# Optimization experiments

Measured on AMD Instinct MI355X. Metric: run time of the kernel, lower is better.

Reference implementation:

```python
import jax, jax.numpy as jnp
import numpy as np

B, S, D, H = 2, 2048, 1024, 16
HD = D // H  # head_dim = 64
SCALE = HD ** -0.5


def setup_inputs() -> dict:
    key = jax.random.key(0)
    ks = jax.random.split(key, 10)
    std = D ** -0.5
    return {
        "x": jax.random.normal(ks[0], (B, S, D), jnp.float32),
        "y": jax.random.normal(ks[1], (B, S, D), jnp.float32),
        "Wq": jax.random.normal(ks[2], (D, D), jnp.float32) * std,
        "bq": jnp.zeros((D,), jnp.float32),
        "Wk": jax.random.normal(ks[3], (D, D), jnp.float32) * std,
        "bk": jnp.zeros((D,), jnp.float32),
        "Wv": jax.random.normal(ks[4], (D, D), jnp.float32) * std,
        "bv": jnp.zeros((D,), jnp.float32),
        "Wo": jax.random.normal(ks[5], (D, D), jnp.float32) * std,
        "bo": jnp.zeros((D,), jnp.float32),
    }


def reference(x, y, Wq, bq, Wk, bk, Wv, bv, Wo, bo):
    # Linear projections (torch Linear: x @ W.T + b; here W stored as [in,out])
    q = x @ Wq + bq  # [B,S,D]
    k = y @ Wk + bk
    v = y @ Wv + bv
    # split heads -> [B,H,S,hd]
    q = q.reshape(B, S, H, HD).transpose(0, 2, 1, 3)
    k = k.reshape(B, S, H, HD).transpose(0, 2, 1, 3)
    v = v.reshape(B, S, H, HD).transpose(0, 2, 1, 3)
    scores = jnp.einsum("bhqd,bhkd->bhqk", q, k) * SCALE  # [B,H,S,S]
    causal = jnp.tril(jnp.ones((S, S), dtype=bool))  # keep lower triangle
    scores = jnp.where(causal[None, None], scores, -jnp.inf)
    attn = jax.nn.softmax(scores, axis=-1)
    out = jnp.einsum("bhqk,bhkd->bhqd", attn, v)  # [B,H,S,hd]
    out = out.transpose(0, 2, 1, 3).reshape(B, S, D)
    return out @ Wo + bo
```

## Files before the change

kernel.cpp:

```cpp
#include <hip/hip_runtime.h>
#include <hip/hip_bf16.h>


#define BDIM 2
#define SDIM 2048
#define DDIM 1024
#define HDIM 16
#define HD   64
#define MDIM (BDIM*SDIM)
#define C2 0.18033688011112042f

using short8  = __attribute__((ext_vector_type(8))) short;
using floatx4 = __attribute__((ext_vector_type(4))) float;

static __device__ __forceinline__ unsigned short f2bf(float x) {
    union { float f; unsigned int u; } c; c.f = x;
    unsigned int r = (c.u + 0x7fffu + ((c.u >> 16) & 1u)) >> 16;
    return (unsigned short)r;
}

static __device__ __forceinline__ unsigned int pack2bf(float a, float b) {
    union { float f; unsigned int u; } ua, ub;
    ua.f = a; ub.f = b;
    return __builtin_amdgcn_perm(ub.u + 0x8000u, ua.u + 0x8000u, 0x07060302u);
}

#define GLD16(g, l) __builtin_amdgcn_global_load_lds(                        \
    (const __attribute__((address_space(1))) void*)(g),                      \
    (__attribute__((address_space(3))) void*)(l), 16, 0, 0)

__global__ __launch_bounds__(256) void prep_kernel(
    const float* __restrict__ X, const float* __restrict__ Y,
    const float* __restrict__ W0, const float* __restrict__ W1,
    const float* __restrict__ W2, const float* __restrict__ W3,
    unsigned short* __restrict__ Xo, unsigned short* __restrict__ Yo,
    unsigned short* __restrict__ T0, unsigned short* __restrict__ T1,
    unsigned short* __restrict__ T2, unsigned short* __restrict__ T3)
{
    __shared__ float tile[64][68];
    const int z = blockIdx.z;
    const int t = threadIdx.x;
    if (z < 2) {
        const float* A    = z ? Y : X;
        unsigned short* O = z ? Yo : Xo;
        const int idx = blockIdx.x * 256 + t;
        const float4 a = ((const float4*)A)[idx*2];
        const float4 b = ((const float4*)A)[idx*2 + 1];
        ushort4 lo, hi;
        lo.x = f2bf(a.x); lo.y = f2bf(a.y); lo.z = f2bf(a.z); lo.w = f2bf(a.w);
        hi.x = f2bf(b.x); hi.y = f2bf(b.y); hi.z = f2bf(b.z); hi.w = f2bf(b.w);
        ((ushort4*)O)[idx*2]     = lo;
        ((ushort4*)O)[idx*2 + 1] = hi;
        return;
    }
    if (blockIdx.x >= 256) return;
    const int zz = z - 2;
    const float* W    = (zz == 0) ? W0 : (zz == 1) ? W1 : (zz == 2) ? W2 : W3;
    unsigned short* T = (zz == 0) ? T0 : (zz == 1) ? T1 : (zz == 2) ? T2 : T3;
    const int k0 = (blockIdx.x & 15) * 64, n0 = (blockIdx.x >> 4) * 64;
    #pragma unroll
    for (int i = 0; i < 4; ++i) {
        const int idx = t + i*256;
        const int kr = idx >> 4, c4 = idx & 15;
        float4 v = *(const float4*)&W[(size_t)(k0 + kr) * DDIM + n0 + c4*4];
        tile[kr][c4*4+0] = v.x; tile[kr][c4*4+1] = v.y;
        tile[kr][c4*4+2] = v.z; tile[kr][c4*4+3] = v.w;
    }
    __syncthreads();
    #pragma unroll
    for (int i = 0; i < 4; ++i) {
        const int idx = t + i*256;
        const int nr = idx >> 4, kc = idx & 15;
        ushort4 o;
        o.x = f2bf(tile[kc*4+0][nr]); o.y = f2bf(tile[kc*4+1][nr]);
        o.z = f2bf(tile[kc*4+2][nr]); o.w = f2bf(tile[kc*4+3][nr]);
        *(ushort4*)&T[(size_t)(n0 + nr) * DDIM + k0 + kc*4] = o;
    }
}

template <bool SWAP>
__device__ __forceinline__ void gemm128_core(
    const unsigned short* __restrict__ A, const unsigned short* __restrict__ Bt,
    int bm, int bn, unsigned short* As, unsigned short* Bs, floatx4 acc[4][4])
{
    const int t = threadIdx.x;
    const int w = t >> 6, l = t & 63;
    const int quad = l >> 4, col = l & 15;
    const int wr = (w >> 1) * 64, wc = (w & 1) * 64;

    const int c1 = t + 256;
    const int r0 = t >> 2,  o0 = (t & 3) * 8;
    const int r1 = c1 >> 2, o1 = (c1 & 3) * 8;

    const unsigned short* Ar0 = A  + (size_t)(bm + r0) * DDIM + o0;
    const unsigned short* Ar1 = A  + (size_t)(bm + r1) * DDIM + o1;
    const unsigned short* Br0 = Bt + (size_t)(bn + r0) * DDIM + o0;
    const unsigned short* Br1 = Bt + (size_t)(bn + r1) * DDIM + o1;

    GLD16(Ar0, As + t*8);
    GLD16(Ar1, As + c1*8);
    GLD16(Br0, Bs + t*8);
    GLD16(Br1, Bs + c1*8);

    for (int kt = 0; kt < DDIM; kt += 32) {
        const int cur = (kt >> 5) & 1;
        unsigned short* Asn = As + (cur ^ 1) * 4096;
        unsigned short* Bsn = Bs + (cur ^ 1) * 4096;
        __syncthreads();
        if (kt + 32 < DDIM) {
            GLD16(Ar0 + kt + 32, Asn + t*8);
            GLD16(Ar1 + kt + 32, Asn + c1*8);
            GLD16(Br0 + kt + 32, Bsn + t*8);
            GLD16(Br1 + kt + 32, Bsn + c1*8);
        }
        const unsigned short* Asc = As + cur*4096;
        const unsigned short* Bsc = Bs + cur*4096;
        short8 af[4], bfr[4];
        #pragma unroll
        for (int i = 0; i < 4; ++i)
            af[i] = *(const short8*)&Asc[(wr + i*16 + col)*32 + quad*8];
        #pragma unroll
        for (int j = 0; j < 4; ++j)
            bfr[j] = *(const short8*)&Bsc[(wc + j*16 + col)*32 + quad*8];
        #pragma unroll
        for (int i = 0; i < 4; ++i)
            #pragma unroll
            for (int j = 0; j < 4; ++j)
                acc[i][j] = SWAP
                    ? __builtin_amdgcn_mfma_f32_16x16x32_bf16(bfr[j], af[i], acc[i][j], 0, 0, 0)
                    : __builtin_amdgcn_mfma_f32_16x16x32_bf16(af[i], bfr[j], acc[i][j], 0, 0, 0);
    }
}

__global__ __launch_bounds__(256) void qkv_gemm_kernel(
    const unsigned short* __restrict__ xbf, const unsigned short* __restrict__ ybf,
    const unsigned short* __restrict__ Wqt, const unsigned short* __restrict__ Wkt,
    const unsigned short* __restrict__ Wvt,
    const float* __restrict__ bq, const float* __restrict__ bk,
    const float* __restrict__ bv,
    unsigned short* __restrict__ Qbf, unsigned short* __restrict__ Kbf,
    unsigned short* __restrict__ vT)
{
    __shared__ __align__(16) unsigned short As[2*4096];
    __shared__ __align__(16) unsigned short Bs[2*4096];

    const int z = blockIdx.z;
    const unsigned short* A  = (z == 0) ? xbf : ybf;
    const unsigned short* Wt = (z == 0) ? Wqt : (z == 1) ? Wkt : Wvt;
    const float* bp          = (z == 0) ? bq  : (z == 1) ? bk  : bv;

    const int bm = (blockIdx.x * 4 + (blockIdx.y & 3)) * 128;
    const int bn = (blockIdx.y >> 2) * 128;

    const int t = threadIdx.x;
    const int w = t >> 6, l = t & 63;
    const int quad = l >> 4, col = l & 15;
    const int wr = (w >> 1) * 64, wc = (w & 1) * 64;

    floatx4 acc[4][4] = {};

    if (z < 2) {
        gemm128_core<true>(A, Wt, bm, bn, As, Bs, acc);
        unsigned short* O = (z == 0) ? Qbf : Kbf;
        const float sc = (z == 0) ? C2 : 1.0f;
        float4 bias4[4];
        #pragma unroll
        for (int j = 0; j < 4; ++j)
            bias4[j] = *(const float4*)&bp[bn + wc + j*16 + quad*4];
        #pragma unroll
        for (int i = 0; i < 4; ++i) {
            const int m = bm + wr + i*16 + col;
            unsigned short* rowp = O + (size_t)m * DDIM;
            #pragma unroll
            for (int j = 0; j < 4; ++j) {
                const float v0 = (acc[i][j][0] + bias4[j].x) * sc;
                const float v1 = (acc[i][j][1] + bias4[j].y) * sc;
                const float v2 = (acc[i][j][2] + bias4[j].z) * sc;
                const float v3 = (acc[i][j][3] + bias4[j].w) * sc;
                uint2 pk;
                pk.x = pack2bf(v0, v1);
                pk.y = pack2bf(v2, v3);
                *(uint2*)&rowp[bn + wc + j*16 + quad*4] = pk;
            }
        }
    } else {
        gemm128_core<false>(A, Wt, bm, bn, As, Bs, acc);
        #pragma unroll
        for (int j = 0; j < 4; ++j) {
            const int gn = bn + wc + j*16 + col;
            const float bias = bp[gn];
            #pragma unroll
            for (int i = 0; i < 4; ++i) {
                const int gm0 = bm + wr + i*16 + quad*4;
                uint2 pk;
                pk.x = pack2bf(acc[i][j][0] + bias, acc[i][j][1] + bias);
                pk.y = pack2bf(acc[i][j][2] + bias, acc[i][j][3] + bias);
                *(uint2*)&vT[((size_t)((gm0 >> 11) * DDIM + gn)) * SDIM + (gm0 & 2047)] = pk;
            }
        }
    }
}

__global__ __launch_bounds__(256) void out_gemm_kernel(
    const unsigned short* __restrict__ Obf, const unsigned short* __restrict__ Wot,
    const float* __restrict__ bo, float* __restrict__ out)
{
    __shared__ __align__(16) unsigned short As[2*4096];
    __shared__ __align__(16) unsigned short Bs[2*2048];

    const int t = threadIdx.x;
    const int w = t >> 6, l = t & 63;
    const int quad = l >> 4, col = l & 15;

    const int j  = (blockIdx.x >> 3) + 2 * blockIdx.y;
    const int bm = ((blockIdx.x & 7) * 4 + (j & 3)) * 128;
    const int bn = (j >> 2) * 64;

    const int wr = (w >> 1) * 64, wc = (w & 1) * 32;

    const int r0 = t >> 2, o0 = (t & 3) * 8;
    const unsigned short* Ar0 = Obf + (size_t)(bm + r0) * DDIM + o0;
    const unsigned short* Ar1 = Obf + (size_t)(bm + 64 + r0) * DDIM + o0;
    const unsigned short* Br  = Wot + (size_t)(bn + r0) * DDIM + o0;

    floatx4 acc[4][2] = {};

    GLD16(Ar0, As + t*8);
    GLD16(Ar1, As + (t + 256)*8);
    GLD16(Br,  Bs + t*8);

    for (int kt = 0; kt < DDIM; kt += 32) {
        const int cur = (kt >> 5) & 1;
        unsigned short* Asn = As + (cur ^ 1) * 4096;
        unsigned short* Bsn = Bs + (cur ^ 1) * 2048;
        __syncthreads();
        if (kt + 32 < DDIM) {
            GLD16(Ar0 + kt + 32, Asn + t*8);
            GLD16(Ar1 + kt + 32, Asn + (t + 256)*8);
            GLD16(Br  + kt + 32, Bsn + t*8);
        }
        const unsigned short* Asc = As + cur*4096;
        const unsigned short* Bsc = Bs + cur*2048;
        short8 af[4], bfr[2];
        #pragma unroll
        for (int i = 0; i < 4; ++i)
            af[i] = *(const short8*)&Asc[(wr + i*16 + col)*32 + quad*8];
        #pragma unroll
        for (int j2 = 0; j2 < 2; ++j2)
            bfr[j2] = *(const short8*)&Bsc[(wc + j2*16 + col)*32 + quad*8];
        #pragma unroll
        for (int i = 0; i < 4; ++i)
            #pragma unroll
            for (int j2 = 0; j2 < 2; ++j2)
                acc[i][j2] = __builtin_amdgcn_mfma_f32_16x16x32_bf16(
                    bfr[j2], af[i], acc[i][j2], 0, 0, 0);
    }

    float4 bias4[2];
    #pragma unroll
    for (int j2 = 0; j2 < 2; ++j2)
        bias4[j2] = *(const float4*)&bo[bn + wc + j2*16 + quad*4];
    #pragma unroll
    for (int i = 0; i < 4; ++i) {
        const int m = bm + wr + i*16 + col;
        float* rowp = out + (size_t)m * DDIM;
        #pragma unroll
        for (int j2 = 0; j2 < 2; ++j2) {
            float4 o;
            o.x = acc[i][j2][0] + bias4[j2].x;
            o.y = acc[i][j2][1] + bias4[j2].y;
            o.z = acc[i][j2][2] + bias4[j2].z;
            o.w = acc[i][j2][3] + bias4[j2].w;
            *(float4*)&rowp[bn + wc + j2*16 + quad*4] = o;
        }
    }
}

__global__ __launch_bounds__(256, 4) void attn_mfma_kernel(
    const unsigned short* __restrict__ Qbf, const unsigned short* __restrict__ Kbf,
    const unsigned short* __restrict__ vT, unsigned short* __restrict__ Obf)
{
    __shared__ __align__(16) unsigned short KfL[2][512*8];
    __shared__ __align__(16) unsigned short VfL[2][512*8];
    __shared__ __align__(16) unsigned short PfL[4*1024];

    const int t = threadIdx.x;
    const int w = t >> 6, l = t & 63;
    const int quad = l >> 4, col = l & 15;
    const int h  = blockIdx.x, b = blockIdx.z;
    const int qt = b ? (31 - blockIdx.y) : blockIdx.y;
    const size_t hoff = (size_t)h * HD;
    const size_t bS = (size_t)b * SDIM;
    const size_t bD = (size_t)b * DDIM;

    const int qwb = qt * 64 + w * 16;
    const int nk_block = qt + 1;

    const unsigned short* kp[2];
    const unsigned short* vp[2];
    int kdst[2], vdst[2];
    #pragma unroll
    for (int i = 0; i < 2; ++i) {
        const int f = 2*w + i;
        kp[i]   = Kbf + (bS + (f >> 1)*16 + col) * DDIM + hoff + (f & 1)*32 + quad*8;
        vp[i]   = vT  + (bD + hoff + (f >> 1)*16 + col) * SDIM + (f & 1)*32 + quad*8;
        kdst[i] = (f*64 + l)*8;
        vdst[i] = (f*64 + l)*8;
    }

    short8 qf[2];
    #pragma unroll
    for (int kc = 0; kc < 2; ++kc)
        qf[kc] = *(const short8*)
            &Qbf[(bS + qwb + col) * DDIM + hoff + kc*32 + quad*8];

    float lrun = 0.0f;
    floatx4 o[4] = {};

    #pragma unroll
    for (int i = 0; i < 2; ++i) {
        GLD16(kp[i], &KfL[0][kdst[i]]);
        GLD16(vp[i], &VfL[0][vdst[i]]);
    }

    #pragma unroll 1
    for (int it = 0; it < nk_block; ++it) {
        const int ktb = it * 64;
        const int cur = it & 1;
        __syncthreads();
        if (it + 1 < nk_block) {
            const int nxt = cur ^ 1;
            const size_t ko = (size_t)(it + 1) * 64 * DDIM;
            const int    vo = (it + 1) * 64;
            #pragma unroll
            for (int i = 0; i < 2; ++i) {
                GLD16(kp[i] + ko, &KfL[nxt][kdst[i]]);
                GLD16(vp[i] + vo, &VfL[nxt][vdst[i]]);
            }
        }

        const unsigned short* Kb = KfL[cur];
        const unsigned short* Vb = VfL[cur];
        short8 kf[4][2], vfr[4][2];
        #pragma unroll
        for (int kt = 0; kt < 4; ++kt)
            #pragma unroll
            for (int kc = 0; kc < 2; ++kc)
                kf[kt][kc] = *(const short8*)&Kb[((kt*2 + kc)*64 + l)*8];
        #pragma unroll
        for (int n = 0; n < 4; ++n)
            #pragma unroll
            for (int kk = 0; kk < 2; ++kk)
                vfr[n][kk] = *(const short8*)&Vb[((n*2 + kk)*64 + l)*8];

        floatx4 sT[4];
        __builtin_amdgcn_s_setprio(1);
        #pragma unroll
        for (int kt = 0; kt < 4; ++kt) {
            floatx4 z = {};
            z = __builtin_amdgcn_mfma_f32_16x16x32_bf16(kf[kt][0], qf[0], z, 0, 0, 0);
            z = __builtin_amdgcn_mfma_f32_16x16x32_bf16(kf[kt][1], qf[1], z, 0, 0, 0);
            sT[kt] = z;
        }
        __builtin_amdgcn_s_setprio(0);

        const int qrow = qwb + col;
        const bool anymask = (ktb + 63 > qwb);
        float p[4][4];
        #pragma unroll
        for (int kt = 0; kt < 4; ++kt)
            #pragma unroll
            for (int r = 0; r < 4; ++r) {
                float xv = sT[kt][r];
                if (anymask && (ktb + kt*16 + quad*4 + r > qrow))
                    xv = -1e30f;
                p[kt][r] = exp2f(xv);
            }

        float st[4];
        #pragma unroll
        for (int kt = 0; kt < 4; ++kt)
            st[kt] = (p[kt][0] + p[kt][1]) + (p[kt][2] + p[kt][3]);
        lrun += (st[0] + st[1]) + (st[2] + st[3]);

        const int pb = w * 1024;
        #pragma unroll
        for (int kt = 0; kt < 4; ++kt) {
            uint2 pk;
            pk.x = pack2bf(p[kt][0], p[kt][1]);
            pk.y = pack2bf(p[kt][2], p[kt][3]);
            *(uint2*)&PfL[pb + ((kt*2 + (quad>>1))*16 + col)*8 + (quad&1)*4] = pk;
        }
        const short8 pf0 = *(const short8*)&PfL[pb + ((0*4 + quad)*16 + col)*8];
        const short8 pf1 = *(const short8*)&PfL[pb + ((1*4 + quad)*16 + col)*8];
        __builtin_amdgcn_s_setprio(1);
        #pragma unroll
        for (int n = 0; n < 4; ++n) {
            o[n] = __builtin_amdgcn_mfma_f32_16x16x32_bf16(vfr[n][0], pf0, o[n], 0, 0, 0);
            o[n] = __builtin_amdgcn_mfma_f32_16x16x32_bf16(vfr[n][1], pf1, o[n], 0, 0, 0);
        }
        __builtin_amdgcn_s_setprio(0);
    }

    float lt = lrun;
    lt += __shfl_xor(lt, 16);
    lt += __shfl_xor(lt, 32);
    const float inv = 1.0f / lt;
    #pragma unroll
    for (int n = 0; n < 4; ++n) {
        ushort4 pk;
        pk.x = f2bf(o[n][0] * inv); pk.y = f2bf(o[n][1] * inv);
        pk.z = f2bf(o[n][2] * inv); pk.w = f2bf(o[n][3] * inv);
        *(ushort4*)&Obf[(bS + qwb + col) * DDIM + hoff + n*16 + quad*4] = pk;
    }
}

extern "C" void kernel_launch(void* const* d_in, const int* in_sizes, int n_in,
                              void* d_out, int out_size, void* d_ws, size_t ws_size,
                              hipStream_t stream) {
    const float* x  = (const float*)d_in[0];
    const float* y  = (const float*)d_in[1];
    const float* Wq = (const float*)d_in[2];
    const float* bq = (const float*)d_in[3];
    const float* Wk = (const float*)d_in[4];
    const float* bk = (const float*)d_in[5];
    const float* Wv = (const float*)d_in[6];
    const float* bv = (const float*)d_in[7];
    const float* Wo = (const float*)d_in[8];
    const float* bo = (const float*)d_in[9];
    float* out = (float*)d_out;

    const size_t mat  = (size_t)MDIM * DDIM;
    const size_t wmat = (size_t)DDIM * DDIM;
    unsigned short* p = (unsigned short*)d_ws;
    unsigned short* xbf = p;            p += mat;
    unsigned short* ybf = p;            p += mat;
    unsigned short* Wqt = p;            p += wmat;
    unsigned short* Wkt = p;            p += wmat;
    unsigned short* Wvt = p;            p += wmat;
    unsigned short* Wot = p;            p += wmat;
    unsigned short* Qbf = p;            p += mat;
    unsigned short* Kbf = p;            p += mat;
    unsigned short* vT  = p;            p += mat;
    unsigned short* Obf = p;            p += mat;

    hipLaunchKernelGGL(prep_kernel, dim3(MDIM*DDIM/8/256, 1, 6), dim3(256),
                       0, stream, x, y, Wq, Wk, Wv, Wo,
                       xbf, ybf, Wqt, Wkt, Wvt, Wot);

    hipLaunchKernelGGL(qkv_gemm_kernel, dim3(DDIM/128, MDIM/128, 3), dim3(256),
                       0, stream, xbf, ybf, Wqt, Wkt, Wvt, bq, bk, bv,
                       Qbf, Kbf, vT);

    hipLaunchKernelGGL(attn_mfma_kernel, dim3(16, 32, BDIM), dim3(256),
                       0, stream, Qbf, Kbf, vT, Obf);

    hipLaunchKernelGGL(out_gemm_kernel, dim3(DDIM/64, MDIM/128), dim3(256),
                       0, stream, Obf, Wot, bo, out);
}
```

Measured before the change: 218.2 us.

## Split attention KV range across waves with register-resident P and LDS reduction

```diff
diff --git a/kernel.cpp b/kernel.cpp
--- a/kernel.cpp
+++ b/kernel.cpp
@@ -276,142 +276,158 @@
     }
 }
 
-__global__ __launch_bounds__(256, 4) void attn_mfma_kernel(
+__global__ __launch_bounds__(256, 2) void attn_mfma_kernel(
     const unsigned short* __restrict__ Qbf, const unsigned short* __restrict__ Kbf,
     const unsigned short* __restrict__ vT, unsigned short* __restrict__ Obf)
 {
-    __shared__ __align__(16) unsigned short KfL[2][512*8];
-    __shared__ __align__(16) unsigned short VfL[2][512*8];
-    __shared__ __align__(16) unsigned short PfL[4*1024];
+    __shared__ float ls[2][4*64];
+    __shared__ __align__(16) floatx4 os[2][1024];
 
     const int t = threadIdx.x;
     const int w = t >> 6, l = t & 63;
     const int quad = l >> 4, col = l & 15;
-    const int h  = blockIdx.x, b = blockIdx.z;
-    const int qt = b ? (31 - blockIdx.y) : blockIdx.y;
+
+    const int lin = blockIdx.x;
+    const int j   = lin >> 3, rem = j & 3;
+    const int qt  = 31 - (j >> 2);
+    const int b   = rem & 1;
+    const int h   = (lin & 7) + 8 * (rem >> 1);
+
     const size_t hoff = (size_t)h * HD;
-    const size_t bS = (size_t)b * SDIM;
-    const size_t bD = (size_t)b * DDIM;
-
-    const int qwb = qt * 64 + w * 16;
-    const int nk_block = qt + 1;
-
-    const unsigned short* kp[2];
-    const unsigned short* vp[2];
-    int kdst[2], vdst[2];
+    const size_t bS   = (size_t)b * SDIM;
+    const size_t bD   = (size_t)b * DDIM;
+    const int qb = qt * 64;
+
+    short8 qf[4][2];
     #pragma unroll
-    for (int i = 0; i < 2; ++i) {
-        const int f = 2*w + i;
-        kp[i]   = Kbf + (bS + (f >> 1)*16 + col) * DDIM + hoff + (f & 1)*32 + quad*8;
-        vp[i]   = vT  + (bD + hoff + (f >> 1)*16 + col) * SDIM + (f & 1)*32 + quad*8;
-        kdst[i] = (f*64 + l)*8;
-        vdst[i] = (f*64 + l)*8;
-    }
-
-    short8 qf[2];
-    #pragma unroll
-    for (int kc = 0; kc < 2; ++kc)
-        qf[kc] = *(const short8*)
-            &Qbf[(bS + qwb + col) * DDIM + hoff + kc*32 + quad*8];
-
-    float lrun = 0.0f;
-    floatx4 o[4] = {};
-
-    #pragma unroll
-    for (int i = 0; i < 2; ++i) {
-        GLD16(kp[i], &KfL[0][kdst[i]]);
-        GLD16(vp[i], &VfL[0][vdst[i]]);
-    }
+    for (int m = 0; m < 4; ++m)
+        #pragma unroll
+        for (int hf = 0; hf < 2; ++hf)
+            qf[m][hf] = *(const short8*)
+                &Qbf[(bS + qb + m*16 + col) * DDIM + hoff + hf*32 + quad*8];
+
+    floatx4 o[4][4] = {};
+    float lrun[4] = {0.f, 0.f, 0.f, 0.f};
+
+    const int rowp = ((col >> 2) << 3) | (col & 3);
+    const unsigned short* kb0 = Kbf + bS * DDIM + hoff + quad*8;
+    const unsigned short* vb0 = vT + (bD + hoff + col) * SDIM + quad*8;
 
     #pragma unroll 1
-    for (int it = 0; it < nk_block; ++it) {
+    for (int it = w; it <= qt; it += 4) {
         const int ktb = it * 64;
-        const int cur = it & 1;
-        __syncthreads();
-        if (it + 1 < nk_block) {
-            const int nxt = cur ^ 1;
-            const size_t ko = (size_t)(it + 1) * 64 * DDIM;
-            const int    vo = (it + 1) * 64;
-            #pragma unroll
-            for (int i = 0; i < 2; ++i) {
-                GLD16(kp[i] + ko, &KfL[nxt][kdst[i]]);
-                GLD16(vp[i] + vo, &VfL[nxt][vdst[i]]);
+        const bool diag = (it == qt);
+
+        short8 kf[2][2][2];
+        #pragma unroll
+        for (int c = 0; c < 2; ++c)
+            #pragma unroll
+            for (int tt = 0; tt < 2; ++tt) {
+                const size_t row = (size_t)(ktb + c*32 + tt*4 + rowp);
+                kf[c][tt][0] = *(const short8*)&kb0[row * DDIM];
+                kf[c][tt][1] = *(const short8*)&kb0[row * DDIM + 32];
             }
-        }
-
-        const unsigned short* Kb = KfL[cur];
-        const unsigned short* Vb = VfL[cur];
-        short8 kf[4][2], vfr[4][2];
-        #pragma unroll
-        for (int kt = 0; kt < 4; ++kt)
-            #pragma unroll
-            for (int kc = 0; kc < 2; ++kc)
-                kf[kt][kc] = *(const short8*)&Kb[((kt*2 + kc)*64 + l)*8];
+        short8 vf[4][2];
         #pragma unroll
         for (int n = 0; n < 4; ++n)
             #pragma unroll
-            for (int kk = 0; kk < 2; ++kk)
-                vfr[n][kk] = *(const short8*)&Vb[((n*2 + kk)*64 + l)*8];
-
-        floatx4 sT[4];
-        __builtin_amdgcn_s_setprio(1);
-        #pragma unroll
-        for (int kt = 0; kt < 4; ++kt) {
-            floatx4 z = {};
-            z = __builtin_amdgcn_mfma_f32_16x16x32_bf16(kf[kt][0], qf[0], z, 0, 0, 0);
-            z = __builtin_amdgcn_mfma_f32_16x16x32_bf16(kf[kt][1], qf[1], z, 0, 0, 0);
-            sT[kt] = z;
-        }
-        __builtin_amdgcn_s_setprio(0);
-
-        const int qrow = qwb + col;
-        const bool anymask = (ktb + 63 > qwb);
-        float p[4][4];
-        #pragma unroll
-        for (int kt = 0; kt < 4; ++kt)
-            #pragma unroll
-            for (int r = 0; r < 4; ++r) {
-                float xv = sT[kt][r];
-                if (anymask && (ktb + kt*16 + quad*4 + r > qrow))
-                    xv = -1e30f;
-                p[kt][r] = exp2f(xv);
+            for (int c = 0; c < 2; ++c)
+                vf[n][c] = *(const short8*)
+                    &vb0[(size_t)(n*16) * SDIM + ktb + c*32];
+
+        #pragma unroll
+        for (int m = 0; m < 4; ++m) {
+            #pragma unroll
+            for (int c = 0; c < 2; ++c) {
+                if (diag && (c*32 > m*16 + 15)) continue;
+                const bool needm = diag && (c*32 + 31 > m*16);
+
+                floatx4 s0 = {}, s1 = {};
+                __builtin_amdgcn_s_setprio(1);
+                s0 = __builtin_amdgcn_mfma_f32_16x16x32_bf16(kf[c][0][0], qf[m][0], s0, 0, 0, 0);
+                s0 = __builtin_amdgcn_mfma_f32_16x16x32_bf16(kf[c][0][1], qf[m][1], s0, 0, 0, 0);
+                s1 = __builtin_amdgcn_mfma_f32_16x16x32_bf16(kf[c][1][0], qf[m][0], s1, 0, 0, 0);
+                s1 = __builtin_amdgcn_mfma_f32_16x16x32_bf16(kf[c][1][1], qf[m][1], s1, 0, 0, 0);
+                __builtin_amdgcn_s_setprio(0);
+
+                float p0[4], p1[4];
+                const int qrow = m*16 + col;
+                const int kls  = c*32 + quad*8;
+                #pragma unroll
+                for (int r = 0; r < 4; ++r) {
+                    p0[r] = (needm && (kls + r     > qrow)) ? 0.0f : exp2f(s0[r]);
+                    p1[r] = (needm && (kls + 4 + r > qrow)) ? 0.0f : exp2f(s1[r]);
+                }
+                lrun[m] += ((p0[0]+p0[1]) + (p0[2]+p0[3]))
+                         + ((p1[0]+p1[1]) + (p1[2]+p1[3]));
+
+                union { short8 v; unsigned int u[4]; } pf;
+                pf.u[0] = pack2bf(p0[0], p0[1]);
+                pf.u[1] = pack2bf(p0[2], p0[3]);
+                pf.u[2] = pack2bf(p1[0], p1[1]);
+                pf.u[3] = pack2bf(p1[2], p1[3]);
+
+                __builtin_amdgcn_s_setprio(1);
+                #pragma unroll
+                for (int n = 0; n < 4; ++n)
+                    o[n][m] = __builtin_amdgcn_mfma_f32_16x16x32_bf16(
+                        vf[n][c], pf.v, o[n][m], 0, 0, 0);
+                __builtin_amdgcn_s_setprio(0);
             }
-
-        float st[4];
-        #pragma unroll
-        for (int kt = 0; kt < 4; ++kt)
-            st[kt] = (p[kt][0] + p[kt][1]) + (p[kt][2] + p[kt][3]);
-        lrun += (st[0] + st[1]) + (st[2] + st[3]);
-
-        const int pb = w * 1024;
-        #pragma unroll
-        for (int kt = 0; kt < 4; ++kt) {
-            uint2 pk;
-            pk.x = pack2bf(p[kt][0], p[kt][1]);
-            pk.y = pack2bf(p[kt][2], p[kt][3]);
-            *(uint2*)&PfL[pb + ((kt*2 + (quad>>1))*16 + col)*8 + (quad&1)*4] = pk;
-        }
-        const short8 pf0 = *(const short8*)&PfL[pb + ((0*4 + quad)*16 + col)*8];
-        const short8 pf1 = *(const short8*)&PfL[pb + ((1*4 + quad)*16 + col)*8];
-        __builtin_amdgcn_s_setprio(1);
-        #pragma unroll
-        for (int n = 0; n < 4; ++n) {
-            o[n] = __builtin_amdgcn_mfma_f32_16x16x32_bf16(vfr[n][0], pf0, o[n], 0, 0, 0);
-            o[n] = __builtin_amdgcn_mfma_f32_16x16x32_bf16(vfr[n][1], pf1, o[n], 0, 0, 0);
-        }
-        __builtin_amdgcn_s_setprio(0);
-    }
-
-    float lt = lrun;
-    lt += __shfl_xor(lt, 16);
-    lt += __shfl_xor(lt, 32);
-    const float inv = 1.0f / lt;
-    #pragma unroll
-    for (int n = 0; n < 4; ++n) {
-        ushort4 pk;
-        pk.x = f2bf(o[n][0] * inv); pk.y = f2bf(o[n][1] * inv);
-        pk.z = f2bf(o[n][2] * inv); pk.w = f2bf(o[n][3] * inv);
-        *(ushort4*)&Obf[(bS + qwb + col) * DDIM + hoff + n*16 + quad*4] = pk;
+        }
+    }
+
+    if (w >= 2) {
+        const int s = w - 2;
+        #pragma unroll
+        for (int n = 0; n < 4; ++n)
+            #pragma unroll
+            for (int m = 0; m < 4; ++m)
+                os[s][(n*4 + m)*64 + l] = o[n][m];
+        #pragma unroll
+        for (int m = 0; m < 4; ++m)
+            ls[s][m*64 + l] = lrun[m];
+    }
+    __syncthreads();
+    if (w < 2) {
+        #pragma unroll
+        for (int n = 0; n < 4; ++n)
+            #pragma unroll
+            for (int m = 0; m < 4; ++m)
+                o[n][m] += os[w][(n*4 + m)*64 + l];
+        #pragma unroll
+        for (int m = 0; m < 4; ++m)
+            lrun[m] += ls[w][m*64 + l];
+    }
+    __syncthreads();
+    if (w == 1) {
+        #pragma unroll
+        for (int n = 0; n < 4; ++n)
+            #pragma unroll
+            for (int m = 0; m < 4; ++m)
+                os[0][(n*4 + m)*64 + l] = o[n][m];
+        #pragma unroll
+        for (int m = 0; m < 4; ++m)
+            ls[0][m*64 + l] = lrun[m];
+    }
+    __syncthreads();
+    if (w == 0) {
+        #pragma unroll
+        for (int m = 0; m < 4; ++m) {
+            float lt = lrun[m] + ls[0][m*64 + l];
+            lt += __shfl_xor(lt, 16);
+            lt += __shfl_xor(lt, 32);
+            const float inv = 1.0f / lt;
+            #pragma unroll
+            for (int n = 0; n < 4; ++n) {
+                const floatx4 ov = o[n][m] + os[0][(n*4 + m)*64 + l];
+                uint2 pk;
+                pk.x = pack2bf(ov[0] * inv, ov[1] * inv);
+                pk.y = pack2bf(ov[2] * inv, ov[3] * inv);
+                *(uint2*)&Obf[(bS + qb + m*16 + col) * DDIM
+                              + hoff + n*16 + quad*4] = pk;
+            }
+        }
     }
 }
 
@@ -452,7 +468,7 @@
                        0, stream, xbf, ybf, Wqt, Wkt, Wvt, bq, bk, bv,
                        Qbf, Kbf, vT);
 
-    hipLaunchKernelGGL(attn_mfma_kernel, dim3(16, 32, BDIM), dim3(256),
+    hipLaunchKernelGGL(attn_mfma_kernel, dim3(1024), dim3(256),
                        0, stream, Qbf, Kbf, vT, Obf);
 
     hipLaunchKernelGGL(out_gemm_kernel, dim3(DDIM/64, MDIM/128), dim3(256),
```

New measurement: 208.5 us. 1.05x faster.
